# Kernel optimization log

Measured on AMD Instinct MI355X. Metric: run time of the kernel, lower is better.

The kernel has to match this reference:

```python
import jax, jax.numpy as jnp
import numpy as np

K = 3  # kernel_size
S = 1  # stride
P = 1  # padding


def setup_inputs() -> dict:
    key = jax.random.key(0)
    ks = jax.random.split(key, 5)
    B, C, H, W, O = 4, 64, 128, 128, 64
    x = jax.random.normal(ks[0], (B, C, H, W), jnp.float32)
    # offset conv params (module inits these to 0; use small random values so the
    # bilinear-gather path is actually exercised with non-integer offsets)
    w_off = jax.random.normal(ks[1], (2 * K * K, C, K, K), jnp.float32) * 0.01
    b_off = jax.random.normal(ks[2], (2 * K * K,), jnp.float32) * 0.01
    # deformable conv params (torchvision DeformConv2d has bias=True by default)
    w_dcn = jax.random.normal(ks[3], (O, C, K, K), jnp.float32) * (1.0 / np.sqrt(C * K * K))
    b_dcn = jax.random.normal(ks[4], (O,), jnp.float32) * 0.01
    return {"x": x, "w_off": w_off, "b_off": b_off, "w_dcn": w_dcn, "b_dcn": b_dcn}


def _conv(x, w, b):
    y = jax.lax.conv_general_dilated(
        x, w, window_strides=(S, S), padding=[(P, P), (P, P)],
        dimension_numbers=("NCHW", "OIHW", "NCHW"))
    return y + b[None, :, None, None]


def _deform_conv2d(x, offset, w_dcn, b_dcn):
    # x: [B,C,H,W]; offset: [B, 2*K*K, Ho, Wo] with (dy, dx) interleaved per
    # kernel tap (row-major kh*K+kw), matching torchvision deform_conv2d.
    B, C, H, W = x.shape
    Ho, Wo = offset.shape[2], offset.shape[3]
    K2 = K * K
    off = offset.reshape(B, K2, 2, Ho, Wo)
    oy, ox = off[:, :, 0], off[:, :, 1]  # [B,K2,Ho,Wo]

    kh = (jnp.arange(K2) // K).astype(jnp.float32)
    kw = (jnp.arange(K2) % K).astype(jnp.float32)
    base_y = (jnp.arange(Ho) * S - P).astype(jnp.float32)
    base_x = (jnp.arange(Wo) * S - P).astype(jnp.float32)
    # fractional sampling locations: p0 + p_k + offset
    py = base_y[None, None, :, None] + kh[None, :, None, None] + oy  # [B,K2,Ho,Wo]
    px = base_x[None, None, None, :] + kw[None, :, None, None] + ox

    y0f = jnp.floor(py); x0f = jnp.floor(px)
    dy = py - y0f; dx = px - x0f
    y0 = y0f.astype(jnp.int32); x0 = x0f.astype(jnp.int32)

    def gather(yi, xi):
        # implicit zero padding: mask out-of-range corners
        valid = (yi >= 0) & (yi < H) & (xi >= 0) & (xi < W)
        yc = jnp.clip(yi, 0, H - 1)
        xc = jnp.clip(xi, 0, W - 1)
        v = jax.vmap(lambda xb, yb, xib: xb[:, yb, xib])(x, yc, xc)  # [B,C,K2,Ho,Wo]
        return v * valid[:, None].astype(x.dtype)

    v00 = gather(y0, x0)
    v01 = gather(y0, x0 + 1)
    v10 = gather(y0 + 1, x0)
    v11 = gather(y0 + 1, x0 + 1)

    wy = dy[:, None]; wx = dx[:, None]  # [B,1,K2,Ho,Wo]
    sampled = (v00 * (1 - wy) * (1 - wx) + v01 * (1 - wy) * wx
               + v10 * wy * (1 - wx) + v11 * wy * wx)  # [B,C,K2,Ho,Wo]

    O = w_dcn.shape[0]
    out = jnp.einsum("bckij,ock->boij", sampled, w_dcn.reshape(O, C, K2))
    return out + b_dcn[None, :, None, None]


def reference(x, w_off, b_off, w_dcn, b_dcn):
    offset = _conv(x, w_off, b_off)          # [B, 2*K*K, Ho, Wo]
    return _deform_conv2d(x, offset, w_dcn, b_dcn)
```

## Files before the change

### kernel.cpp

```cpp
#include <hip/hip_runtime.h>
#include <hip/hip_fp16.h>

#define B_ 4
#define H_ 128
#define W_ 128
#define HW_ 16384

typedef _Float16 half8 __attribute__((ext_vector_type(8)));
typedef float floatx4 __attribute__((ext_vector_type(4)));


__global__ __launch_bounds__(256) void k_prep_w(
    const float* __restrict__ w_dcn, const float* __restrict__ w_off,
    __half* __restrict__ W2L, __half* __restrict__ W0L)
{
    int idx = blockIdx.x*256 + threadIdx.x;
    if (idx < 36864) {
        int e = idx & 7, lane = (idx>>3) & 63, og = (idx>>9) & 3;
        int ks = (idx>>11) & 1, tap = idx >> 12;
        int o = og*16 + (lane & 15);
        int c = ks*32 + (lane >> 4)*8 + e;
        W2L[idx] = __float2half(w_dcn[o*576 + c*9 + tap]);
    } else {
        int i2 = idx - 36864;
        int e = i2 & 7, lane = (i2>>3) & 63, h = (i2>>9) & 1;
        int ks = (i2>>10) & 1, tap = i2 >> 11;
        int oc = h*16 + (lane & 15);
        int c = ks*32 + (lane >> 4)*8 + e;
        W0L[i2] = (oc < 18) ? __float2half(w_off[oc*576 + c*9 + tap])
                            : __float2half(0.f);
    }
}

#define CHS2 3488
#define WLOC_OFF 27904
#define SMEM_SZ 37120

__global__ __launch_bounds__(256, 4) void k_fused(
    const float* __restrict__ x, const _Float16* __restrict__ W2L,
    const _Float16* __restrict__ W0L, const float* __restrict__ b_off,
    const float* __restrict__ b_dcn, float* __restrict__ out)
{
    __shared__ __attribute__((aligned(16))) char smem[SMEM_SZ];
    char* halo_c = smem;

    int t = threadIdx.x;
    int lane = t & 63;
    int w = __builtin_amdgcn_readfirstlane(t >> 6);
    int m = lane & 15, q = lane >> 4;

    char*  wl     = smem + WLOC_OFF + w*2304;
    float* offL   = (float*)wl;
    char*  desc   = wl;

    int bid  = blockIdx.x;
    int xcd  = bid & 7, sidx = bid >> 3;
    int orig = xcd*128 + sidx;
    int b    = orig >> 8;
    int rem  = orig & 255;
    int i0   = (rem >> 2) * 2;
    int j0   = (rem & 3) * 32;

    const float* xf = x + (size_t)b * (64*HW_);

    #pragma unroll
    for (int rep = 0; rep < 7; ++rep) {
        int idx = rep*256 + t;
        if (idx < 1728) {
            int ch = idx / 216, pl = idx - ch*216;
            int hr = pl / 36, hx = pl - hr*36;
            int grow = min(max(i0 - 2 + hr, 0), H_-1);
            int gcol = min(max(j0 - 2 + hx, 0), W_-1);
            int gpix = (grow<<7) + gcol;
            const float* s = xf + ch*8*HW_ + gpix;
            half8 v;
            #pragma unroll
            for (int e = 0; e < 8; ++e) v[e] = (_Float16)s[e*HW_];
            *(half8*)(halo_c + ch*CHS2 + pl*16) = v;
        }
    }
    __syncthreads();

    floatx4 accA[2];
    #pragma unroll
    for (int h = 0; h < 2; ++h) accA[h] = (floatx4){0.f,0.f,0.f,0.f};

    const half8 hz = {0,0,0,0,0,0,0,0};
    int pcol = w*16 + m;
    int rA = pcol >> 5, cA = pcol & 31;
    #pragma unroll
    for (int tap = 0; tap < 9; ++tap) {
        int kh = tap/3, kw = tap - (tap/3)*3;
        int ii = i0 + rA - 1 + kh;
        int jj = j0 + cA - 1 + kw;
        bool valid = (ii >= 0) && (ii < H_) && (jj >= 0) && (jj < W_);
        int pixA = (rA + 1 + kh)*36 + (cA + 1 + kw);
        half8 a0 = *(const half8*)(halo_c + q*CHS2     + pixA*16);
        half8 a1 = *(const half8*)(halo_c + (q+4)*CHS2 + pixA*16);
        a0 = valid ? a0 : hz;
        a1 = valid ? a1 : hz;
        #pragma unroll
        for (int ks = 0; ks < 2; ++ks) {
            half8 a = ks ? a1 : a0;
            #pragma unroll
            for (int h = 0; h < 2; ++h) {
                half8 bf = *(const half8*)(W0L + (((tap*2+ks)*2+h)<<9) + (lane<<3));
                accA[h] = __builtin_amdgcn_mfma_f32_16x16x32_f16(a, bf, accA[h], 0, 0, 0);
            }
        }
    }
    #pragma unroll
    for (int h = 0; h < 2; ++h) {
        int oc = h*16 + m;
        if (oc < 18) {
            float bo = b_off[oc];
            #pragma unroll
            for (int r = 0; r < 4; ++r)
                offL[(q*4 + r)*18 + oc] = accA[h][r] + bo;
        }
    }

    uint4 dreg[3];
    #pragma unroll
    for (int e = 0; e < 3; ++e) {
        int idx = e*64 + lane;
        if (idx < 144) {
            int pl  = idx / 9;
            int tap = idx - pl*9;
            int kh = tap/3, kw = tap - (tap/3)*3;
            int pos = w*16 + pl;
            int r = pos >> 5, c = pos & 31;
            float2 o2 = *(const float2*)(offL + pl*18 + 2*tap);
            float py = (float)(i0 + r - 1 + kh) + o2.x;
            float px = (float)(j0 + c - 1 + kw) + o2.y;
            float y0f = floorf(py), x0f = floorf(px);
            float dy = py - y0f, dx = px - x0f;
            int y0 = (int)y0f, x0i = (int)x0f;
            int y1 = y0 + 1,  x1 = x0i + 1;
            bool vy0 = (y0>=0)&(y0<H_),   vy1 = (y1>=0)&(y1<H_);
            bool vx0 = (x0i>=0)&(x0i<W_), vx1 = (x1>=0)&(x1<W_);
            int yc0 = min(max(y0,0),H_-1),  yc1 = min(max(y1,0),H_-1);
            int xc0 = min(max(x0i,0),W_-1), xc1 = min(max(x1,0),W_-1);
            float w00 = (1.f-dy)*(1.f-dx) * ((vy0&&vx0)?1.f:0.f);
            float w01 = (1.f-dy)*dx       * ((vy0&&vx1)?1.f:0.f);
            float w10 = dy*(1.f-dx)       * ((vy1&&vx0)?1.f:0.f);
            float w11 = dy*dx             * ((vy1&&vx1)?1.f:0.f);
            int hy0 = yc0 - (i0-2), hy1 = yc1 - (i0-2);
            int hx0 = xc0 - (j0-2), hx1 = xc1 - (j0-2);
            bool inh = ((unsigned)hy0 < 6u) & ((unsigned)hy1 < 6u)
                     & ((unsigned)hx0 < 36u) & ((unsigned)hx1 < 36u);
            unsigned a0,a1,a2,a3;
            if (inh) { a0 = hy0*36+hx0; a1 = hy0*36+hx1; a2 = hy1*36+hx0; a3 = hy1*36+hx1; }
            else     { a0 = ((yc0<<7)+xc0) | 0x8000u; a1 = (yc0<<7)+xc1;
                       a2 = (yc1<<7)+xc0;             a3 = (yc1<<7)+xc1; }
            __half2 hw0 = __floats2half2_rn(w00, w01);
            __half2 hw1 = __floats2half2_rn(w10, w11);
            dreg[e].x = a0 | (a1 << 16);
            dreg[e].y = a2 | (a3 << 16);
            dreg[e].z = *(unsigned*)&hw0;
            dreg[e].w = *(unsigned*)&hw1;
        }
    }
    #pragma unroll
    for (int e = 0; e < 3; ++e) {
        int idx = e*64 + lane;
        if (idx < 144) *(uint4*)(desc + idx*16) = dreg[e];
    }

    floatx4 acc[4];
    #pragma unroll
    for (int og = 0; og < 4; ++og) acc[og] = (floatx4){0.f,0.f,0.f,0.f};

    const char* hq0 = halo_c + q*CHS2;
    const char* hq1 = halo_c + (q+4)*CHS2;

    #pragma unroll 3
    for (int tap = 0; tap < 9; ++tap) {
        uint4 d = *(const uint4*)(desc + (m*9 + tap)*16);
        unsigned p0i = d.x & 0x7fffu, p1i = d.x >> 16;
        unsigned p2i = d.y & 0xffffu, p3i = d.y >> 16;
        bool inh = (d.x & 0x8000u) == 0u;
        unsigned short b00 = (unsigned short)(d.z & 0xffffu);
        unsigned short b01 = (unsigned short)(d.z >> 16);
        unsigned short b10 = (unsigned short)(d.w & 0xffffu);
        unsigned short b11 = (unsigned short)(d.w >> 16);
        _Float16 h00 = *(_Float16*)&b00, h01 = *(_Float16*)&b01;
        _Float16 h10 = *(_Float16*)&b10, h11 = *(_Float16*)&b11;
        half8 W00 = {h00,h00,h00,h00,h00,h00,h00,h00};
        half8 W01 = {h01,h01,h01,h01,h01,h01,h01,h01};
        half8 W10 = {h10,h10,h10,h10,h10,h10,h10,h10};
        half8 W11 = {h11,h11,h11,h11,h11,h11,h11,h11};
        half8 v00a,v01a,v10a,v11a, v00b,v01b,v10b,v11b;
        if (inh) {
            v00a = *(const half8*)(hq0 + p0i*16);  v00b = *(const half8*)(hq1 + p0i*16);
            v01a = *(const half8*)(hq0 + p1i*16);  v01b = *(const half8*)(hq1 + p1i*16);
            v10a = *(const half8*)(hq0 + p2i*16);  v10b = *(const half8*)(hq1 + p2i*16);
            v11a = *(const half8*)(hq0 + p3i*16);  v11b = *(const half8*)(hq1 + p3i*16);
        } else {
            #pragma unroll
            for (int e = 0; e < 8; ++e) {
                v00a[e] = (_Float16)xf[(q*8+e)*HW_ + (int)p0i];
                v00b[e] = (_Float16)xf[((q+4)*8+e)*HW_ + (int)p0i];
                v01a[e] = (_Float16)xf[(q*8+e)*HW_ + (int)p1i];
                v01b[e] = (_Float16)xf[((q+4)*8+e)*HW_ + (int)p1i];
                v10a[e] = (_Float16)xf[(q*8+e)*HW_ + (int)p2i];
                v10b[e] = (_Float16)xf[((q+4)*8+e)*HW_ + (int)p2i];
                v11a[e] = (_Float16)xf[(q*8+e)*HW_ + (int)p3i];
                v11b[e] = (_Float16)xf[((q+4)*8+e)*HW_ + (int)p3i];
            }
        }
        half8 sk0 = v00a*W00 + v01a*W01 + v10a*W10 + v11a*W11;
        half8 sk1 = v00b*W00 + v01b*W01 + v10b*W10 + v11b*W11;
        #pragma unroll
        for (int og = 0; og < 4; ++og) {
            half8 bf0 = *(const half8*)(W2L + (((tap*2+0)*4+og)<<9) + (lane<<3));
            acc[og] = __builtin_amdgcn_mfma_f32_16x16x32_f16(sk0, bf0, acc[og], 0, 0, 0);
            half8 bf1 = *(const half8*)(W2L + (((tap*2+1)*4+og)<<9) + (lane<<3));
            acc[og] = __builtin_amdgcn_mfma_f32_16x16x32_f16(sk1, bf1, acc[og], 0, 0, 0);
        }
    }
    __syncthreads();

    float* E = (float*)smem;
    #pragma unroll
    for (int og = 0; og < 4; ++og) {
        #pragma unroll
        for (int r = 0; r < 4; ++r)
            E[(w*16 + q*4 + r)*66 + og*16 + m] = acc[og][r];
    }
    __syncthreads();
    int obase = (b*64)*HW_ + i0*W_ + j0;
    int orow = (lane >> 5)*W_ + (lane & 31);
    #pragma unroll
    for (int rep = 0; rep < 16; ++rep) {
        int o = rep*4 + w;
        out[obase + o*HW_ + orow] = E[lane*66 + o] + b_dcn[o];
    }
}

extern "C" void kernel_launch(void* const* d_in, const int* in_sizes, int n_in,
                              void* d_out, int out_size, void* d_ws, size_t ws_size,
                              hipStream_t stream) {
    const float* x     = (const float*)d_in[0];
    const float* w_off = (const float*)d_in[1];
    const float* b_off = (const float*)d_in[2];
    const float* w_dcn = (const float*)d_in[3];
    const float* b_dcn = (const float*)d_in[4];
    float* out = (float*)d_out;

    __half* W2L = (__half*)d_ws;
    __half* W0L = (__half*)((char*)d_ws + 73728);

    k_prep_w<<<216, 256, 0, stream>>>(w_dcn, w_off, W2L, W0L);
    k_fused<<<1024, 256, 0, stream>>>(x, (const _Float16*)W2L,
                                      (const _Float16*)W0L, b_off, b_dcn, out);
}
```

Measured before the change: 96.65 us.

## Switch to 32x32x16 MFMA with two-wave blocks covering one row each

Replaces the 16x16x32 MFMA tiling with 32x32x16 instructions, so each of two waves computes a full 32-pixel row against all 64 output channels (two 32-wide output groups), and reorganizes the prepared weight layouts to match. Blocks shrink from 256 to 128 threads, and each wave now builds sampling descriptors for 32 pixels. The aim is to reuse each bilinearly interpolated A fragment across more output channels and issue fewer MFMA instructions. In exchange, per-thread work and register pressure rise, the halo load loop runs twice as many iterations per thread, and fewer threads share the per-block shared-memory fill.

```diff
diff --git a/kernel.cpp b/kernel.cpp
--- a/kernel.cpp
+++ b/kernel.cpp
@@ -7,7 +7,7 @@
 #define HW_ 16384
 
 typedef _Float16 half8 __attribute__((ext_vector_type(8)));
-typedef float floatx4 __attribute__((ext_vector_type(4)));
+typedef float floatx16 __attribute__((ext_vector_type(16)));
 
 
 __global__ __launch_bounds__(256) void k_prep_w(
@@ -16,17 +16,17 @@
 {
     int idx = blockIdx.x*256 + threadIdx.x;
     if (idx < 36864) {
-        int e = idx & 7, lane = (idx>>3) & 63, og = (idx>>9) & 3;
-        int ks = (idx>>11) & 1, tap = idx >> 12;
-        int o = og*16 + (lane & 15);
-        int c = ks*32 + (lane >> 4)*8 + e;
+        int e = idx & 7, lane = (idx>>3) & 63, og = (idx>>9) & 1;
+        int ks = (idx>>10) & 3, tap = idx >> 12;
+        int o = og*32 + (lane & 31);
+        int c = ks*16 + (lane >> 5)*8 + e;
         W2L[idx] = __float2half(w_dcn[o*576 + c*9 + tap]);
     } else {
         int i2 = idx - 36864;
-        int e = i2 & 7, lane = (i2>>3) & 63, h = (i2>>9) & 1;
-        int ks = (i2>>10) & 1, tap = i2 >> 11;
-        int oc = h*16 + (lane & 15);
-        int c = ks*32 + (lane >> 4)*8 + e;
+        int e = i2 & 7, lane = (i2>>3) & 63;
+        int ks = (i2>>9) & 3, tap = i2 >> 11;
+        int oc = lane & 31;
+        int c = ks*16 + (lane >> 5)*8 + e;
         W0L[i2] = (oc < 18) ? __float2half(w_off[oc*576 + c*9 + tap])
                             : __float2half(0.f);
     }
@@ -36,7 +36,7 @@
 #define WLOC_OFF 27904
 #define SMEM_SZ 37120
 
-__global__ __launch_bounds__(256, 4) void k_fused(
+__global__ __launch_bounds__(128, 2) void k_fused(
     const float* __restrict__ x, const _Float16* __restrict__ W2L,
     const _Float16* __restrict__ W0L, const float* __restrict__ b_off,
     const float* __restrict__ b_dcn, float* __restrict__ out)
@@ -46,12 +46,13 @@
 
     int t = threadIdx.x;
     int lane = t & 63;
-    int w = __builtin_amdgcn_readfirstlane(t >> 6);
-    int m = lane & 15, q = lane >> 4;
-
-    char*  wl     = smem + WLOC_OFF + w*2304;
-    float* offL   = (float*)wl;
-    char*  desc   = wl;
+    int v = __builtin_amdgcn_readfirstlane(t >> 6);
+    int c31 = lane & 31;
+    int h8  = lane >> 5;
+
+    char*  wl   = smem + WLOC_OFF + v*4608;
+    float* offL = (float*)wl;
+    char*  desc = wl;
 
     int bid  = blockIdx.x;
     int xcd  = bid & 7, sidx = bid >> 3;
@@ -63,9 +64,8 @@
 
     const float* xf = x + (size_t)b * (64*HW_);
 
-    #pragma unroll
-    for (int rep = 0; rep < 7; ++rep) {
-        int idx = rep*256 + t;
+    for (int rep = 0; rep < 14; ++rep) {
+        int idx = rep*128 + t;
         if (idx < 1728) {
             int ch = idx / 216, pl = idx - ch*216;
             int hr = pl / 36, hx = pl - hr*36;
@@ -73,66 +73,61 @@
             int gcol = min(max(j0 - 2 + hx, 0), W_-1);
             int gpix = (grow<<7) + gcol;
             const float* s = xf + ch*8*HW_ + gpix;
-            half8 v;
+            half8 vv;
             #pragma unroll
-            for (int e = 0; e < 8; ++e) v[e] = (_Float16)s[e*HW_];
-            *(half8*)(halo_c + ch*CHS2 + pl*16) = v;
+            for (int e = 0; e < 8; ++e) vv[e] = (_Float16)s[e*HW_];
+            *(half8*)(halo_c + ch*CHS2 + pl*16) = vv;
         }
     }
     __syncthreads();
 
-    floatx4 accA[2];
-    #pragma unroll
-    for (int h = 0; h < 2; ++h) accA[h] = (floatx4){0.f,0.f,0.f,0.f};
-
+    floatx16 accA = {0.f,0.f,0.f,0.f,0.f,0.f,0.f,0.f,0.f,0.f,0.f,0.f,0.f,0.f,0.f,0.f};
     const half8 hz = {0,0,0,0,0,0,0,0};
-    int pcol = w*16 + m;
-    int rA = pcol >> 5, cA = pcol & 31;
     #pragma unroll
     for (int tap = 0; tap < 9; ++tap) {
         int kh = tap/3, kw = tap - (tap/3)*3;
-        int ii = i0 + rA - 1 + kh;
-        int jj = j0 + cA - 1 + kw;
+        int ii = i0 + v - 1 + kh;
+        int jj = j0 + c31 - 1 + kw;
         bool valid = (ii >= 0) && (ii < H_) && (jj >= 0) && (jj < W_);
-        int pixA = (rA + 1 + kh)*36 + (cA + 1 + kw);
-        half8 a0 = *(const half8*)(halo_c + q*CHS2     + pixA*16);
-        half8 a1 = *(const half8*)(halo_c + (q+4)*CHS2 + pixA*16);
-        a0 = valid ? a0 : hz;
-        a1 = valid ? a1 : hz;
+        int pixA = (v + 1 + kh)*36 + (c31 + 1 + kw);
         #pragma unroll
-        for (int ks = 0; ks < 2; ++ks) {
-            half8 a = ks ? a1 : a0;
-            #pragma unroll
-            for (int h = 0; h < 2; ++h) {
-                half8 bf = *(const half8*)(W0L + (((tap*2+ks)*2+h)<<9) + (lane<<3));
-                accA[h] = __builtin_amdgcn_mfma_f32_16x16x32_f16(a, bf, accA[h], 0, 0, 0);
-            }
-        }
-    }
-    #pragma unroll
-    for (int h = 0; h < 2; ++h) {
-        int oc = h*16 + m;
+        for (int s = 0; s < 4; ++s) {
+            half8 a = *(const half8*)(halo_c + (s*2 + h8)*CHS2 + pixA*16);
+            a = valid ? a : hz;
+            half8 bf = *(const half8*)(W0L + ((tap*4+s)<<9) + (lane<<3));
+            accA = __builtin_amdgcn_mfma_f32_32x32x16_f16(a, bf, accA, 0, 0, 0);
+        }
+    }
+    {
+        int oc = c31;
         if (oc < 18) {
             float bo = b_off[oc];
             #pragma unroll
-            for (int r = 0; r < 4; ++r)
-                offL[(q*4 + r)*18 + oc] = accA[h][r] + bo;
-        }
-    }
-
-    uint4 dreg[3];
-    #pragma unroll
-    for (int e = 0; e < 3; ++e) {
+            for (int r = 0; r < 16; ++r) {
+                int row = (r & 3) + 8*(r >> 2) + 4*h8;
+                offL[row*18 + oc] = accA[r] + bo;
+            }
+        }
+    }
+
+    float2 o2r[5];
+    #pragma unroll
+    for (int e = 0; e < 5; ++e) {
         int idx = e*64 + lane;
-        if (idx < 144) {
-            int pl  = idx / 9;
-            int tap = idx - pl*9;
+        if (idx < 288) {
+            int pl = idx / 9, tap = idx - pl*9;
+            o2r[e] = *(const float2*)(offL + pl*18 + 2*tap);
+        }
+    }
+    uint4 dreg[5];
+    #pragma unroll
+    for (int e = 0; e < 5; ++e) {
+        int idx = e*64 + lane;
+        if (idx < 288) {
+            int pl = idx / 9, tap = idx - pl*9;
             int kh = tap/3, kw = tap - (tap/3)*3;
-            int pos = w*16 + pl;
-            int r = pos >> 5, c = pos & 31;
-            float2 o2 = *(const float2*)(offL + pl*18 + 2*tap);
-            float py = (float)(i0 + r - 1 + kh) + o2.x;
-            float px = (float)(j0 + c - 1 + kw) + o2.y;
+            float py = (float)(i0 + v - 1 + kh) + o2r[e].x;
+            float px = (float)(j0 + pl - 1 + kw) + o2r[e].y;
             float y0f = floorf(py), x0f = floorf(px);
             float dy = py - y0f, dx = px - x0f;
             int y0 = (int)y0f, x0i = (int)x0f;
@@ -162,21 +157,25 @@
         }
     }
     #pragma unroll
-    for (int e = 0; e < 3; ++e) {
+    for (int e = 0; e < 5; ++e) {
         int idx = e*64 + lane;
-        if (idx < 144) *(uint4*)(desc + idx*16) = dreg[e];
-    }
-
-    floatx4 acc[4];
-    #pragma unroll
-    for (int og = 0; og < 4; ++og) acc[og] = (floatx4){0.f,0.f,0.f,0.f};
-
-    const char* hq0 = halo_c + q*CHS2;
-    const char* hq1 = halo_c + (q+4)*CHS2;
+        if (idx < 288) {
+            int pl = idx / 9, tap = idx - pl*9;
+            *(uint4*)(desc + (tap*32 + pl)*16) = dreg[e];
+        }
+    }
+
+    floatx16 acc0 = {0.f,0.f,0.f,0.f,0.f,0.f,0.f,0.f,0.f,0.f,0.f,0.f,0.f,0.f,0.f,0.f};
+    floatx16 acc1 = acc0;
+
+    const char* hqs0 = halo_c + (0*2 + h8)*CHS2;
+    const char* hqs1 = halo_c + (1*2 + h8)*CHS2;
+    const char* hqs2 = halo_c + (2*2 + h8)*CHS2;
+    const char* hqs3 = halo_c + (3*2 + h8)*CHS2;
 
     #pragma unroll 3
     for (int tap = 0; tap < 9; ++tap) {
-        uint4 d = *(const uint4*)(desc + (m*9 + tap)*16);
+        uint4 d = *(const uint4*)(desc + (tap*32 + c31)*16);
         unsigned p0i = d.x & 0x7fffu, p1i = d.x >> 16;
         unsigned p2i = d.y & 0xffffu, p3i = d.y >> 16;
         bool inh = (d.x & 0x8000u) == 0u;
@@ -190,51 +189,53 @@
         half8 W01 = {h01,h01,h01,h01,h01,h01,h01,h01};
         half8 W10 = {h10,h10,h10,h10,h10,h10,h10,h10};
         half8 W11 = {h11,h11,h11,h11,h11,h11,h11,h11};
-        half8 v00a,v01a,v10a,v11a, v00b,v01b,v10b,v11b;
-        if (inh) {
-            v00a = *(const half8*)(hq0 + p0i*16);  v00b = *(const half8*)(hq1 + p0i*16);
-            v01a = *(const half8*)(hq0 + p1i*16);  v01b = *(const half8*)(hq1 + p1i*16);
-            v10a = *(const half8*)(hq0 + p2i*16);  v10b = *(const half8*)(hq1 + p2i*16);
-            v11a = *(const half8*)(hq0 + p3i*16);  v11b = *(const half8*)(hq1 + p3i*16);
-        } else {
-            #pragma unroll
-            for (int e = 0; e < 8; ++e) {
-                v00a[e] = (_Float16)xf[(q*8+e)*HW_ + (int)p0i];
-                v00b[e] = (_Float16)xf[((q+4)*8+e)*HW_ + (int)p0i];
-                v01a[e] = (_Float16)xf[(q*8+e)*HW_ + (int)p1i];
-                v01b[e] = (_Float16)xf[((q+4)*8+e)*HW_ + (int)p1i];
-                v10a[e] = (_Float16)xf[(q*8+e)*HW_ + (int)p2i];
-                v10b[e] = (_Float16)xf[((q+4)*8+e)*HW_ + (int)p2i];
-                v11a[e] = (_Float16)xf[(q*8+e)*HW_ + (int)p3i];
-                v11b[e] = (_Float16)xf[((q+4)*8+e)*HW_ + (int)p3i];
+        half8 sk[4];
+        const char* hb[4] = {hqs0, hqs1, hqs2, hqs3};
+        #pragma unroll
+        for (int s = 0; s < 4; ++s) {
+            half8 v00, v01, v10, v11;
+            if (inh) {
+                v00 = *(const half8*)(hb[s] + p0i*16);
+                v01 = *(const half8*)(hb[s] + p1i*16);
+                v10 = *(const half8*)(hb[s] + p2i*16);
+                v11 = *(const half8*)(hb[s] + p3i*16);
+            } else {
+                int chb = (s*2 + h8)*8;
+                #pragma unroll
+                for (int e = 0; e < 8; ++e) {
+                    v00[e] = (_Float16)xf[(chb+e)*HW_ + (int)p0i];
+                    v01[e] = (_Float16)xf[(chb+e)*HW_ + (int)p1i];
+                    v10[e] = (_Float16)xf[(chb+e)*HW_ + (int)p2i];
+                    v11[e] = (_Float16)xf[(chb+e)*HW_ + (int)p3i];
+                }
             }
-        }
-        half8 sk0 = v00a*W00 + v01a*W01 + v10a*W10 + v11a*W11;
-        half8 sk1 = v00b*W00 + v01b*W01 + v10b*W10 + v11b*W11;
+            sk[s] = v00*W00 + v01*W01 + v10*W10 + v11*W11;
+        }
         #pragma unroll
-        for (int og = 0; og < 4; ++og) {
-            half8 bf0 = *(const half8*)(W2L + (((tap*2+0)*4+og)<<9) + (lane<<3));
-            acc[og] = __builtin_amdgcn_mfma_f32_16x16x32_f16(sk0, bf0, acc[og], 0, 0, 0);
-            half8 bf1 = *(const half8*)(W2L + (((tap*2+1)*4+og)<<9) + (lane<<3));
-            acc[og] = __builtin_amdgcn_mfma_f32_16x16x32_f16(sk1, bf1, acc[og], 0, 0, 0);
+        for (int s = 0; s < 4; ++s) {
+            half8 bf0 = *(const half8*)(W2L + (((tap*4+s)*2+0)<<9) + (lane<<3));
+            acc0 = __builtin_amdgcn_mfma_f32_32x32x16_f16(sk[s], bf0, acc0, 0, 0, 0);
+            half8 bf1 = *(const half8*)(W2L + (((tap*4+s)*2+1)<<9) + (lane<<3));
+            acc1 = __builtin_amdgcn_mfma_f32_32x32x16_f16(sk[s], bf1, acc1, 0, 0, 0);
         }
     }
     __syncthreads();
 
     float* E = (float*)smem;
     #pragma unroll
-    for (int og = 0; og < 4; ++og) {
-        #pragma unroll
-        for (int r = 0; r < 4; ++r)
-            E[(w*16 + q*4 + r)*66 + og*16 + m] = acc[og][r];
+    for (int r = 0; r < 16; ++r) {
+        int row = (r & 3) + 8*(r >> 2) + 4*h8;
+        int pl  = v*32 + row;
+        E[pl*66 + c31]      = acc0[r];
+        E[pl*66 + 32 + c31] = acc1[r];
     }
     __syncthreads();
     int obase = (b*64)*HW_ + i0*W_ + j0;
-    int orow = (lane >> 5)*W_ + (lane & 31);
-    #pragma unroll
-    for (int rep = 0; rep < 16; ++rep) {
-        int o = rep*4 + w;
-        out[obase + o*HW_ + orow] = E[lane*66 + o] + b_dcn[o];
+    int prow = (lane >> 5)*W_ + c31;
+    #pragma unroll
+    for (int rep = 0; rep < 32; ++rep) {
+        int o = rep*2 + v;
+        out[obase + o*HW_ + prow] = E[lane*66 + o] + b_dcn[o];
     }
 }
 
@@ -252,6 +253,6 @@
     __half* W0L = (__half*)((char*)d_ws + 73728);
 
     k_prep_w<<<216, 256, 0, stream>>>(w_dcn, w_off, W2L, W0L);
-    k_fused<<<1024, 256, 0, stream>>>(x, (const _Float16*)W2L,
+    k_fused<<<1024, 128, 0, stream>>>(x, (const _Float16*)W2L,
                                       (const _Float16*)W0L, b_off, b_dcn, out);
 }
```

Result: faster. 94.47 us (-2.3%).
